# Optimization experiments

Measured on AMD Instinct MI355X. Metric: run time of the kernel, lower is better.

## Reference

```python
import jax, jax.numpy as jnp
import numpy as np

M_CHK, N_VAR, DV = 576, 1152, 3  # (3,x)-regular-column LDPC, rate 1/2
PI = 3.1415926


def _build_bp_matrices():
    """Vectorized replica of GetMatrixForBPNet (same math, no Python O(E^2) loops)."""
    rng = np.random.default_rng(0)
    H = np.zeros((M_CHK, N_VAR), np.float32)
    rows = np.argsort(rng.random((N_VAR, M_CHK)), axis=1)[:, :DV]  # DV distinct rows per column
    H[rows.ravel(), np.repeat(np.arange(N_VAR), DV)] = 1.0
    ii, jj = np.nonzero(H)                 # row-major edge list (sorted by row, then col)
    E = ii.size
    p_r2l = np.lexsort((ii, jj))           # Map_row_to_line: col-major position -> row-major index
    p_l2r = np.argsort(p_r2l)              # Map_line_to_row: inverse permutation
    cols_cm = jj[p_r2l]                    # column of each edge in col-major ("line") order
    # variable-node sum excluding self, in col-major order, then permute row-major input -> col-major
    S_V = (cols_cm[:, None] == cols_cm[None, :]).astype(np.float32)
    np.fill_diagonal(S_V, 0.0)
    H_sumV_to_C = np.zeros((E, E), np.float32)
    H_sumV_to_C[:, p_r2l] = S_V
    # check-node sum excluding self, in row-major order, then permute col-major input -> row-major
    S_C = (ii[:, None] == ii[None, :]).astype(np.float32)
    np.fill_diagonal(S_C, 0.0)
    H_sumC_to_V = np.zeros((E, E), np.float32)
    H_sumC_to_V[:, p_l2r] = S_C
    # llr -> per-edge init (col-major order)
    H_x_to_xe0 = np.zeros((E, N_VAR), np.float32)
    H_x_to_xe0[np.arange(E), cols_cm] = 1.0
    # per-variable sum of final edge messages (row-major input -> col-major sum)
    A = (np.arange(N_VAR)[:, None] == cols_cm[None, :]).astype(np.float32)
    H_xe_v_sumc_to_y = np.zeros((N_VAR, E), np.float32)
    H_xe_v_sumc_to_y[:, p_r2l] = A
    return H_x_to_xe0, H_sumC_to_V, H_sumV_to_C, H_xe_v_sumc_to_y


def setup_inputs() -> dict:
    key = jax.random.key(0)
    H_x_to_xe0, H_sumC_to_V, H_sumV_to_C, H_xe_v_sumc_to_y = _build_bp_matrices()
    llr_in = 2.0 * jax.random.normal(key, (16, N_VAR), dtype=jnp.float32)
    return {
        "llr_in": llr_in,
        "H_x_to_xe0": jnp.asarray(H_x_to_xe0),
        "H_sumC_to_V": jnp.asarray(H_sumC_to_V),
        "H_sumV_to_C": jnp.asarray(H_sumV_to_C),
        "H_xe_v_sumc_to_y": jnp.asarray(H_xe_v_sumc_to_y),
        "bp_iter_num": 8,
    }


def _one_bp_iteration(xe_v2c, xe_0, H_sumC_to_V, H_sumV_to_C):
    xe_tanh = jnp.tanh(xe_v2c / 2.0)
    sgn = jnp.sign(xe_tanh)
    # log-domain product over check-node neighbors (excluding self) via complex log trick
    sum_log_img = H_sumC_to_V @ ((1.0 - sgn) * (0.5 * PI))
    sum_log_real = H_sumC_to_V @ jnp.log(1e-8 + jnp.abs(xe_tanh))
    xe_product = jnp.exp(sum_log_real) * jnp.cos(sum_log_img)  # Re(exp(r + i*theta))
    xe_pd = xe_product + jnp.sign(xe_product) * (-2e-7)
    # 2 * atanh(x) with the module's custom atanh = 0.5*log((1+x)/(1-x+1e-10))
    xe_v_sumc = jnp.log((1.0 + xe_pd) / (1.0 - xe_pd + 1e-10))
    xe_c_sumv = xe_0 + H_sumV_to_C @ xe_v_sumc
    return xe_v_sumc, xe_c_sumv


def reference(llr_in, H_x_to_xe0, H_sumC_to_V, H_sumV_to_C, H_xe_v_sumc_to_y, bp_iter_num):
    llr_t = llr_in.T                      # [n, batch]
    xe_0 = H_x_to_xe0 @ llr_t             # [E, batch]
    xe_v2c = xe_0
    for _ in range(bp_iter_num - 1):
        _, xe_v2c = _one_bp_iteration(xe_v2c, xe_0, H_sumC_to_V, H_sumV_to_C)
    xe_v_sumc, _ = _one_bp_iteration(xe_v2c, xe_0, H_sumC_to_V, H_sumV_to_C)
    bp_out_llr = llr_t + H_xe_v_sumc_to_y @ xe_v_sumc
    dec_out = (1 - jnp.sign(bp_out_llr).astype(jnp.int32)) // 2
    return dec_out.T
```

## Files before the change

### kernel.cpp

```cpp
#include <hip/hip_runtime.h>

#define NV 1152
#define MC 576
#define NE 3456
#define RPG 36
#define GRP 16
#define EMAX 384

__global__ __launch_bounds__(256) void k_tri(const float* __restrict__ Hy,
                                             unsigned short* __restrict__ pl2r) {
    __shared__ int found[8];
    __shared__ int fcnt;
    const int v = blockIdx.x, t = threadIdx.x;
    if (t == 0) fcnt = 0;
    __syncthreads();
    const float4* row4 = (const float4*)(Hy + (size_t)v * NE);
    for (int c4 = t; c4 < 864; c4 += 256) {
        float4 q = row4[c4];
        if (q.x != 0.0f) { int s = atomicAdd(&fcnt, 1); if (s < 8) found[s] = 4 * c4; }
        if (q.y != 0.0f) { int s = atomicAdd(&fcnt, 1); if (s < 8) found[s] = 4 * c4 + 1; }
        if (q.z != 0.0f) { int s = atomicAdd(&fcnt, 1); if (s < 8) found[s] = 4 * c4 + 2; }
        if (q.w != 0.0f) { int s = atomicAdd(&fcnt, 1); if (s < 8) found[s] = 4 * c4 + 3; }
    }
    __syncthreads();
    if (t == 0) {
        int a = found[0], b2 = found[1], c2 = found[2];
        int lo = min(a, min(b2, c2));
        int hi = max(a, max(b2, c2));
        int mid = a + b2 + c2 - lo - hi;
        pl2r[lo]  = (unsigned short)(3 * v);
        pl2r[mid] = (unsigned short)(3 * v + 1);
        pl2r[hi]  = (unsigned short)(3 * v + 2);
    }
}

__global__ __launch_bounds__(1024) void k_build(const float* __restrict__ Hc,
                                                const unsigned short* __restrict__ pl2r,
                                                uint2* __restrict__ etab) {
    __shared__ unsigned short flg[NE];
    __shared__ int wtot[16];
    __shared__ int rsl[MC + 1];
    const int t = threadIdx.x;
    const int lane = t & 63, wid = t >> 6;
    for (int s = t; s < GRP * EMAX; s += 1024) etab[s] = make_uint2(0u, 0u);
    for (int r = t; r < MC + 1; r += 1024) rsl[r] = NE;
    for (int a = t; a < NE; a += 1024) {
        int fl = 0;
        if (a > 0) fl = (Hc[(size_t)(a - 1) * NE + (int)pl2r[a]] == 0.0f) ? 1 : 0;
        flg[a] = (unsigned short)fl;
    }
    __syncthreads();
    int inc[4];
    int run = 0;
    const int base4 = t * 4;
    #pragma unroll
    for (int k = 0; k < 4; k++) {
        int idx = base4 + k;
        run += (idx < NE) ? (int)flg[idx] : 0;
        inc[k] = run;
    }
    int x = run;
    #pragma unroll
    for (int d = 1; d < 64; d <<= 1) {
        int y = __shfl_up(x, d, 64);
        if (lane >= d) x += y;
    }
    if (lane == 63) wtot[wid] = x;
    __syncthreads();
    if (t < 16) {
        int v = wtot[t];
        #pragma unroll
        for (int d = 1; d < 16; d <<= 1) {
            int y = __shfl_up(v, d, 16);
            if (t >= d) v += y;
        }
        wtot[t] = v;
    }
    __syncthreads();
    const int prefix = ((wid > 0) ? wtot[wid - 1] : 0) + (x - run);
    #pragma unroll
    for (int k = 0; k < 4; k++) {
        int idx = base4 + k;
        if (idx < NE) {
            int rid = prefix + inc[k];
            if (idx == 0 || flg[idx]) rsl[rid] = idx;
        }
    }
    __syncthreads();
    #pragma unroll
    for (int k = 0; k < 4; k++) {
        int a = base4 + k;
        if (a < NE) {
            int r = prefix + inc[k];
            int js = rsl[r];
            int len = rsl[r + 1] - js;
            int g = r / RPG;
            int s0g = rsl[g * RPG];
            int e = pl2r[a];
            int v3 = 3 * (e / 3), r_ = e - v3;
            int o1 = v3 + ((r_ == 0) ? 1 : 0);
            int o2 = v3 + ((r_ == 2) ? 1 : 2);
            etab[g * EMAX + (a - s0g)] =
                make_uint2((unsigned)(e | ((js - s0g) << 16)),
                           (unsigned)(o1 | (o2 << 12) | (len << 24)));
        }
    }
}

__global__ __launch_bounds__(EMAX) void k_iter(const float* __restrict__ llr,
                                               const uint2* __restrict__ etab,
                                               const float* __restrict__ mi,
                                               float* __restrict__ mo,
                                               int first) {
    __shared__ float2 lrli[EMAX];
    const int g = blockIdx.x, b = blockIdx.y, t = threadIdx.x;
    uint2 u = etab[g * EMAX + t];
    const int e   = u.x & 0xFFFF;
    const int jsr = u.x >> 16;
    const int o1  = u.y & 0xFFF;
    const int o2  = (u.y >> 12) & 0xFFF;
    const int len = u.y >> 24;
    if (len) {
        float xv = llr[b * NV + e / 3];
        if (!first) xv = xv + (mi[b * NE + o1] + mi[b * NE + o2]);
        float tv = tanhf(0.5f * xv);
        float sgn = (tv > 0.0f) ? 1.0f : ((tv < 0.0f) ? -1.0f : 0.0f);
        lrli[t] = make_float2(logf(1e-8f + fabsf(tv)),
                              (1.0f - sgn) * 1.5707963f);
    }
    __syncthreads();
    if (len) {
        float slr = 0.0f, sli = 0.0f;
        const int je = jsr + len;
        for (int j = jsr; j < je; ++j) {
            if (j != t) { float2 q = lrli[j]; slr += q.x; sli += q.y; }
        }
        float p = expf(slr) * cosf(sli);
        float ps = (p > 0.0f) ? 1.0f : ((p < 0.0f) ? -1.0f : 0.0f);
        float pd = p - 2e-7f * ps;
        mo[b * NE + e] = logf((1.0f + pd) / ((1.0f - pd) + 1e-10f));
    }
}

__global__ void k_out(const float* __restrict__ llr, const float* __restrict__ msg,
                      int* __restrict__ out, int n) {
    int i = blockIdx.x * 256 + threadIdx.x;
    if (i >= n) return;
    int b = i / NV, v = i - b * NV;
    const float* m = msg + (size_t)b * NE + 3 * v;
    float S = (m[0] + m[1]) + m[2];
    out[i] = ((llr[i] + S) < 0.0f) ? 1 : 0;
}

extern "C" void kernel_launch(void* const* d_in, const int* in_sizes, int n_in,
                              void* d_out, int out_size, void* d_ws, size_t ws_size,
                              hipStream_t stream) {
    const float* llr_in = (const float*)d_in[0];
    const float* Hc2v   = (const float*)d_in[2];
    const float* Hy     = (const float*)d_in[4];
    const int batch = in_sizes[0] / NV;

    uint2* etab = (uint2*)d_ws;
    float* msgA = (float*)(etab + GRP * EMAX);
    float* msgB = msgA + (size_t)batch * NE;
    unsigned short* pl2r = (unsigned short*)(msgB + (size_t)batch * NE);

    hipLaunchKernelGGL(k_tri, dim3(NV), dim3(256), 0, stream, Hy, pl2r);
    hipLaunchKernelGGL(k_build, dim3(1), dim3(1024), 0, stream, Hc2v, pl2r, etab);
    hipLaunchKernelGGL(k_iter, dim3(GRP, batch), dim3(EMAX), 0, stream,
                       llr_in, etab, msgA, msgA, 1);
    float* bufs[2] = { msgA, msgB };
    for (int it = 1; it < 8; ++it) {
        float* in  = bufs[(it + 1) & 1];
        float* out = bufs[it & 1];
        hipLaunchKernelGGL(k_iter, dim3(GRP, batch), dim3(EMAX), 0, stream,
                           llr_in, etab, in, out, 0);
    }
    const int n = batch * NV;
    hipLaunchKernelGGL(k_out, dim3((n + 255) / 256), dim3(256), 0, stream,
                       llr_in, msgB, (int*)d_out, n);
}
```

Measured before the change: 173.8 us.

## Fuse output kernel into last BP iteration and cache per-slot llr in workspace

Removes the separate k_out launch by having the last block of the final k_iter launch, detected through an atomic counter, compute the hard decisions. It also stores each slot's initial llr in a slot-ordered buffer on the first iteration, so later iterations read it contiguously instead of gathering llr[e/3]. The cost is a fence and an atomic per block on the last launch, plus a serial tail where one 384-thread block computes the whole output.

```diff
diff --git a/kernel.cpp b/kernel.cpp
--- a/kernel.cpp
+++ b/kernel.cpp
@@ -6,12 +6,15 @@
 #define RPG 36
 #define GRP 16
 #define EMAX 384
+#define NSLOT (GRP * EMAX)
 
 __global__ __launch_bounds__(256) void k_tri(const float* __restrict__ Hy,
-                                             unsigned short* __restrict__ pl2r) {
+                                             unsigned short* __restrict__ pl2r,
+                                             int* __restrict__ cnt) {
     __shared__ int found[8];
     __shared__ int fcnt;
     const int v = blockIdx.x, t = threadIdx.x;
+    if (v == 0 && t == 0) *cnt = 0;
     if (t == 0) fcnt = 0;
     __syncthreads();
     const float4* row4 = (const float4*)(Hy + (size_t)v * NE);
@@ -42,7 +45,7 @@
     __shared__ int rsl[MC + 1];
     const int t = threadIdx.x;
     const int lane = t & 63, wid = t >> 6;
-    for (int s = t; s < GRP * EMAX; s += 1024) etab[s] = make_uint2(0u, 0u);
+    for (int s = t; s < NSLOT; s += 1024) etab[s] = make_uint2(0u, 0u);
     for (int r = t; r < MC + 1; r += 1024) rsl[r] = NE;
     for (int a = t; a < NE; a += 1024) {
         int fl = 0;
@@ -109,20 +112,33 @@
 
 __global__ __launch_bounds__(EMAX) void k_iter(const float* __restrict__ llr,
                                                const uint2* __restrict__ etab,
+                                               float* __restrict__ x0p,
                                                const float* __restrict__ mi,
                                                float* __restrict__ mo,
-                                               int first) {
+                                               int* __restrict__ out,
+                                               int* __restrict__ cnt,
+                                               int first, int last) {
     __shared__ float2 lrli[EMAX];
+    __shared__ int amlast;
     const int g = blockIdx.x, b = blockIdx.y, t = threadIdx.x;
-    uint2 u = etab[g * EMAX + t];
+    const int slot = g * EMAX + t;
+    uint2 u = etab[slot];
     const int e   = u.x & 0xFFFF;
     const int jsr = u.x >> 16;
-    const int o1  = u.y & 0xFFF;
-    const int o2  = (u.y >> 12) & 0xFFF;
     const int len = u.y >> 24;
     if (len) {
-        float xv = llr[b * NV + e / 3];
-        if (!first) xv = xv + (mi[b * NE + o1] + mi[b * NE + o2]);
+        float xv;
+        if (first) {
+            xv = llr[b * NV + e / 3];
+            x0p[b * NSLOT + slot] = xv;
+        } else {
+            const int o1 = u.y & 0xFFF;
+            const int o2 = (u.y >> 12) & 0xFFF;
+            float x0 = x0p[b * NSLOT + slot];
+            float a1 = mi[b * NE + o1];
+            float a2 = mi[b * NE + o2];
+            xv = x0 + (a1 + a2);
+        }
         float tv = tanhf(0.5f * xv);
         float sgn = (tv > 0.0f) ? 1.0f : ((tv < 0.0f) ? -1.0f : 0.0f);
         lrli[t] = make_float2(logf(1e-8f + fabsf(tv)),
@@ -140,16 +156,25 @@
         float pd = p - 2e-7f * ps;
         mo[b * NE + e] = logf((1.0f + pd) / ((1.0f - pd) + 1e-10f));
     }
-}
-
-__global__ void k_out(const float* __restrict__ llr, const float* __restrict__ msg,
-                      int* __restrict__ out, int n) {
-    int i = blockIdx.x * 256 + threadIdx.x;
-    if (i >= n) return;
-    int b = i / NV, v = i - b * NV;
-    const float* m = msg + (size_t)b * NE + 3 * v;
-    float S = (m[0] + m[1]) + m[2];
-    out[i] = ((llr[i] + S) < 0.0f) ? 1 : 0;
+    if (last) {
+        __threadfence();
+        __syncthreads();
+        if (t == 0) {
+            int old = __hip_atomic_fetch_add(cnt, 1, __ATOMIC_ACQ_REL,
+                                             __HIP_MEMORY_SCOPE_AGENT);
+            amlast = (old == (int)(gridDim.x * gridDim.y) - 1) ? 1 : 0;
+        }
+        __syncthreads();
+        if (amlast) {
+            const int n = (int)gridDim.y * NV;
+            for (int i = t; i < n; i += EMAX) {
+                int bb = i / NV, v = i - bb * NV;
+                const float* m = mo + (size_t)bb * NE + 3 * v;
+                float S = (m[0] + m[1]) + m[2];
+                out[i] = ((llr[i] + S) < 0.0f) ? 1 : 0;
+            }
+        }
+    }
 }
 
 extern "C" void kernel_launch(void* const* d_in, const int* in_sizes, int n_in,
@@ -161,22 +186,22 @@
     const int batch = in_sizes[0] / NV;
 
     uint2* etab = (uint2*)d_ws;
-    float* msgA = (float*)(etab + GRP * EMAX);
+    float* x0p  = (float*)(etab + NSLOT);
+    float* msgA = x0p + (size_t)batch * NSLOT;
     float* msgB = msgA + (size_t)batch * NE;
     unsigned short* pl2r = (unsigned short*)(msgB + (size_t)batch * NE);
-
-    hipLaunchKernelGGL(k_tri, dim3(NV), dim3(256), 0, stream, Hy, pl2r);
+    int* cnt = (int*)(pl2r + NE);
+
+    hipLaunchKernelGGL(k_tri, dim3(NV), dim3(256), 0, stream, Hy, pl2r, cnt);
     hipLaunchKernelGGL(k_build, dim3(1), dim3(1024), 0, stream, Hc2v, pl2r, etab);
     hipLaunchKernelGGL(k_iter, dim3(GRP, batch), dim3(EMAX), 0, stream,
-                       llr_in, etab, msgA, msgA, 1);
+                       llr_in, etab, x0p, msgA, msgA, (int*)d_out, cnt, 1, 0);
     float* bufs[2] = { msgA, msgB };
     for (int it = 1; it < 8; ++it) {
         float* in  = bufs[(it + 1) & 1];
         float* out = bufs[it & 1];
         hipLaunchKernelGGL(k_iter, dim3(GRP, batch), dim3(EMAX), 0, stream,
-                           llr_in, etab, in, out, 0);
-    }
-    const int n = batch * NV;
-    hipLaunchKernelGGL(k_out, dim3((n + 255) / 256), dim3(256), 0, stream,
-                       llr_in, msgB, (int*)d_out, n);
-}
+                           llr_in, etab, x0p, in, out, (int*)d_out, cnt,
+                           0, (it == 7) ? 1 : 0);
+    }
+}
```

Measured after the change: 226.1 us. +30.1%, slower.
